# Optimization experiments

Hardware: AMD Instinct MI355X
Metric: run time of the kernel (lower is better)

The kernel has to match this reference:

```python
import jax, jax.numpy as jnp
import numpy as np
from jax.scipy.linalg import expm

N, T, IN, C, M = 64, 2048, 8, 2, 10  # batch, time, input_size, channels, hidden_size


def setup_inputs() -> dict:
    key = jax.random.key(0)
    k1, k2 = jax.random.split(key)
    x = jax.random.normal(k1, (N, T, IN), dtype=jnp.float32)
    # Lie-algebra generator parameters; small init keeps expm well-conditioned
    A = jax.random.normal(k2, (C, IN, M, M), dtype=jnp.float32) * (1.0 / (M * IN))
    return {"x": x, "A": A}


def dyadic_prod(X):
    # X: (N, T, C, m, m) -> cumulative (ordered) matrix product over time: (N, C, m, m)
    n, t, c, m, _ = X.shape
    levels = int(np.ceil(np.log2(t)))
    I = jnp.broadcast_to(jnp.eye(m, dtype=X.dtype), (n, 1, c, m, m))
    for _ in range(levels):
        if X.shape[1] % 2 == 1:
            X = jnp.concatenate([X, I], axis=1)  # pad with identity
        Xp = X.reshape(n, -1, 2, c, m, m)
        X = jnp.einsum('ntcij,ntcjk->ntcik', Xp[:, :, 0], Xp[:, :, 1])
    return X[:, 0]


def reference(x, A):
    # Skew-symmetrize generators -> so(m) Lie algebra elements, per channel/input dim
    skew = A - jnp.swapaxes(A, -1, -2)          # (C, IN, m, m)
    dX = x[:, 1:] - x[:, :-1]                   # (N, T-1, IN) path increments
    G = jnp.einsum('nti,cijk->ntcjk', dX, skew) # (N, T-1, C, m, m)
    Mexp = expm(G)                              # batched matrix exponential -> SO(m)
    return dyadic_prod(Mexp)                    # (N, C, m, m)
```

## Files before the change

### kernel.cpp

```cpp
#include <hip/hip_runtime.h>

#define NB     64
#define TT     2048
#define INQ    8
#define CC     2
#define MM     10
#define ROWP   12
#define MATS   124
#define SKST   12
#define BLK    512
#define SEGS   96
#define SLEN   11
#define NCHK   2
#define NCHAIN (NB*CC)
#define SLOT   120

typedef float v2f __attribute__((ext_vector_type(2)));

static_assert(SEGS * MATS >= 97 * SLOT, "scratch overlay must fit tree buffer");

__device__ __forceinline__ constexpr int triIdx(int k, int j) {
    return k * 10 + j - ((k + 1) * (k + 2)) / 2;
}

__device__ __forceinline__ void trow_pk(const float* __restrict__ Tri,
                                        v2f* A, v2f* R, const v2f* S, float cj) {
    v2f t[MM];
    t[0] = -S[1] * Tri[triIdx(0, 1)];
    #pragma unroll
    for (int j = 1; j < MM; ++j) t[j] = S[0] * Tri[triIdx(0, j)];
    #pragma unroll
    for (int k = 1; k < MM; ++k) {
        const v2f a = S[k];
        #pragma unroll
        for (int j = 0; j < MM; ++j) {
            if (k == j) continue;
            if (j == 0 && k == 1) continue;
            if (j > k) t[j] += a * Tri[triIdx(k, j)];
            else       t[j] -= a * Tri[triIdx(j, k)];
        }
    }
    #pragma unroll
    for (int j = 0; j < MM; ++j) { A[j] = t[j]; R[j] += cj * t[j]; }
}

__device__ __forceinline__ void taylor5(const float* __restrict__ Tri, v2f* R01) {
    __builtin_amdgcn_s_setprio(1);
    v2f A01[MM];
    trow_pk(Tri, A01, R01, R01, 1.0f);
    trow_pk(Tri, A01, R01, A01, 0.5f);
    trow_pk(Tri, A01, R01, A01, 0.16666667f);
    trow_pk(Tri, A01, R01, A01, 0.041666668f);
    trow_pk(Tri, A01, R01, A01, 0.0083333338f);
    __builtin_amdgcn_s_setprio(0);
}

__device__ __forceinline__ void compute_tvv(const float4* __restrict__ px, int t,
                                            const float4* __restrict__ sg,
                                            float* __restrict__ tvv) {
    const int tc = (t     > TT - 1) ? TT - 1 : t;
    const int t1 = (t + 1 > TT - 1) ? TT - 1 : t + 1;
    const float4 a0 = px[2 * tc], a1 = px[2 * tc + 1];
    const float4 b0 = px[2 * t1], b1 = px[2 * t1 + 1];
    float dx[INQ];
    dx[0] = b0.x - a0.x; dx[1] = b0.y - a0.y;
    dx[2] = b0.z - a0.z; dx[3] = b0.w - a0.w;
    dx[4] = b1.x - a1.x; dx[5] = b1.y - a1.y;
    dx[6] = b1.z - a1.z; dx[7] = b1.w - a1.w;
    #pragma unroll
    for (int i = 0; i < 9; ++i) {
        const float4 s0 = sg[2 * i];
        const float4 s1 = sg[2 * i + 1];
        tvv[i] = dx[0] * s0.x + dx[1] * s0.y + dx[2] * s0.z + dx[3] * s0.w
               + dx[4] * s1.x + dx[5] * s1.y + dx[6] * s1.z + dx[7] * s1.w;
    }
}

__device__ __forceinline__ void store_tvv(float* __restrict__ dst, int r,
                                          const float* __restrict__ tvv) {
    *reinterpret_cast<float4*>(dst + 12 * r)     = make_float4(tvv[0], tvv[1], tvv[2], tvv[3]);
    *reinterpret_cast<float4*>(dst + 12 * r + 4) = make_float4(tvv[4], tvv[5], tvv[6], tvv[7]);
    dst[12 * r + 8] = tvv[8];
}

__device__ __forceinline__ void load_tri(const float* __restrict__ src,
                                         float* __restrict__ Tri) {
    #pragma unroll
    for (int q2 = 0; q2 < 5; ++q2) {
        const float4 u0 = *reinterpret_cast<const float4*>(src + 12 * q2);
        const float4 u1 = *reinterpret_cast<const float4*>(src + 12 * q2 + 4);
        const float  u2 = src[12 * q2 + 8];
        Tri[9 * q2 + 0] = u0.x; Tri[9 * q2 + 1] = u0.y;
        Tri[9 * q2 + 2] = u0.z; Tri[9 * q2 + 3] = u0.w;
        Tri[9 * q2 + 4] = u1.x; Tri[9 * q2 + 5] = u1.y;
        Tri[9 * q2 + 6] = u1.z; Tri[9 * q2 + 7] = u1.w;
        Tri[9 * q2 + 8] = u2;
    }
}

__device__ __forceinline__ void pair_combine(float* buf_s, int ls, int rs, int pq) {
    float lrow[5][MM];
    #pragma unroll
    for (int r = 0; r < 5; ++r) {
        const float4* lr = reinterpret_cast<const float4*>(
            &buf_s[ls * MATS + (pq * 5 + r) * ROWP]);
        const float4 a = lr[0], b = lr[1], c4 = lr[2];
        lrow[r][0] = a.x;  lrow[r][1] = a.y;  lrow[r][2] = a.z;  lrow[r][3] = a.w;
        lrow[r][4] = b.x;  lrow[r][5] = b.y;  lrow[r][6] = b.z;  lrow[r][7] = b.w;
        lrow[r][8] = c4.x; lrow[r][9] = c4.y;
    }
    float d[5][MM];
    #pragma unroll
    for (int r = 0; r < 5; ++r)
        #pragma unroll
        for (int j = 0; j < MM; ++j)
            d[r][j] = 0.0f;
    #pragma unroll
    for (int k = 0; k < MM; ++k) {
        const float4* rr = reinterpret_cast<const float4*>(&buf_s[rs * MATS + k * ROWP]);
        const float4 a = rr[0], b = rr[1], c4 = rr[2];
        float rrow[MM];
        rrow[0] = a.x;  rrow[1] = a.y;  rrow[2] = a.z;  rrow[3] = a.w;
        rrow[4] = b.x;  rrow[5] = b.y;  rrow[6] = b.z;  rrow[7] = b.w;
        rrow[8] = c4.x; rrow[9] = c4.y;
        #pragma unroll
        for (int r = 0; r < 5; ++r) {
            const float lv = lrow[r][k];
            #pragma unroll
            for (int j = 0; j < MM; ++j)
                d[r][j] += lv * rrow[j];
        }
    }
    float* dst = &buf_s[ls * MATS + pq * 5 * ROWP];
    #pragma unroll
    for (int r = 0; r < 5; ++r) {
        float4* drow = reinterpret_cast<float4*>(dst + r * ROWP);
        drow[0] = make_float4(d[r][0], d[r][1], d[r][2], d[r][3]);
        drow[1] = make_float4(d[r][4], d[r][5], d[r][6], d[r][7]);
        drow[2] = make_float4(d[r][8], d[r][9], 0.0f, 0.0f);
    }
}

__global__ __launch_bounds__(BLK, 1)
void dev_serial(const float* __restrict__ x,
                const float* __restrict__ A,
                float* __restrict__ ws)
{
    __shared__ __align__(16) float skq_s[45 * SKST];
    __shared__ __align__(16) float buf_s[SEGS * MATS];

    const int tid   = threadIdx.x;
    const int chain = blockIdx.x >> 1;
    const int qt    = blockIdx.x & 1;
    const int n     = chain >> 1;
    const int c     = chain & 1;

    if (tid < 45 * 8) {
        const int e  = tid >> 3;
        const int ip = tid & 7;
        int k = 0, r2 = e;
        while (r2 >= 9 - k) { r2 -= (9 - k); ++k; }
        const int j = k + 1 + r2;
        const float* Ab = A + (size_t)(c * INQ + ip) * (MM * MM);
        skq_s[e * SKST + ip] = Ab[k * MM + j] - Ab[j * MM + k];
    }
    __syncthreads();

    const int wv  = tid >> 6;
    const int wl  = tid & 63;
    const int g   = wl / 5;
    const int r   = wl - 5 * g;
    const bool act = (wl < 60);
    const int seg = wv * 12 + g;
    const int p0  = 2 * r;

    float4 sg[18];
    {
        const float* srow = &skq_s[(9 * r) * SKST];
        #pragma unroll
        for (int i = 0; i < 9; ++i) {
            sg[2 * i]     = *reinterpret_cast<const float4*>(srow + i * SKST);
            sg[2 * i + 1] = *reinterpret_cast<const float4*>(srow + i * SKST + 4);
        }
    }

    float* slot  = &buf_s[seg * SLOT];
    float* slotw = act ? slot : &buf_s[96 * SLOT];

    v2f R01[MM];
    #pragma unroll
    for (int j = 0; j < MM; ++j)
        R01[j] = (v2f){ (j == p0) ? 1.0f : 0.0f, (j == p0 + 1) ? 1.0f : 0.0f };

    const float4* px = reinterpret_cast<const float4*>(x + (size_t)n * TT * INQ);
    const int t0 = qt * (SEGS * SLEN) + seg * SLEN;

    float tvv[9];
    compute_tvv(px, t0, sg, tvv);
    store_tvv(slotw, r, tvv);

    #pragma unroll 1
    for (int s = 0; s < SLEN - 1; ++s) {
        const int rpar = (s & 1) * 60;
        float Tri[45];
        load_tri(slot + rpar, Tri);
        compute_tvv(px, t0 + s + 1, sg, tvv);
        store_tvv(slotw + (60 - rpar), r, tvv);
        taylor5(Tri, R01);
    }
    {
        float Tri[45];
        load_tri(slot + ((SLEN - 1) & 1) * 60, Tri);
        taylor5(Tri, R01);
    }

    __syncthreads();

    if (act) {
        float* dst = &buf_s[seg * MATS];
        float4* d0 = reinterpret_cast<float4*>(dst + p0 * ROWP);
        d0[0] = make_float4(R01[0].x, R01[1].x, R01[2].x, R01[3].x);
        d0[1] = make_float4(R01[4].x, R01[5].x, R01[6].x, R01[7].x);
        d0[2] = make_float4(R01[8].x, R01[9].x, 0.0f, 0.0f);
        float4* d1 = reinterpret_cast<float4*>(dst + (p0 + 1) * ROWP);
        d1[0] = make_float4(R01[0].y, R01[1].y, R01[2].y, R01[3].y);
        d1[1] = make_float4(R01[4].y, R01[5].y, R01[6].y, R01[7].y);
        d1[2] = make_float4(R01[8].y, R01[9].y, 0.0f, 0.0f);
    }
    __syncthreads();

    #pragma unroll 1
    for (int span = 2; span <= 32; span <<= 1) {
        const int np = SEGS / span;
        if (tid < 2 * np) {
            const int pr = tid >> 1;
            const int pq = tid & 1;
            pair_combine(buf_s, pr * span, pr * span + (span >> 1), pq);
        }
        __syncthreads();
    }
    if (tid < 2) pair_combine(buf_s, 0, 32, tid);
    __syncthreads();
    if (tid < 2) pair_combine(buf_s, 0, 64, tid);
    __syncthreads();

    if (tid < 30) {
        const float4 v = reinterpret_cast<const float4*>(buf_s)[tid];
        reinterpret_cast<float4*>(ws)[((size_t)chain * NCHK + qt) * 30 + tid] = v;
    }
}

__global__ __launch_bounds__(256)
void dev_tree2(const float* __restrict__ ws, float* __restrict__ out)
{
    __shared__ __align__(16) float buf_s[2 * MATS];
    const int tid   = threadIdx.x;
    const int chain = blockIdx.x;

    if (tid < 60) {
        const int m  = tid / 30;
        const int o4 = tid - m * 30;
        const float4 v = reinterpret_cast<const float4*>(ws)[((size_t)chain * 2 + m) * 30 + o4];
        reinterpret_cast<float4*>(&buf_s[m * MATS])[o4] = v;
    }
    __syncthreads();

    if (tid < 2)
        pair_combine(buf_s, 0, 1, tid);
    __syncthreads();

    if (tid < 100) {
        const int i = tid / 10;
        const int j = tid - i * 10;
        out[(size_t)chain * 100 + tid] = buf_s[i * ROWP + j];
    }
}

extern "C" void kernel_launch(void* const* d_in, const int* in_sizes, int n_in,
                              void* d_out, int out_size, void* d_ws, size_t ws_size,
                              hipStream_t stream) {
    (void)in_sizes; (void)n_in; (void)out_size; (void)ws_size;
    const float* x = (const float*)d_in[0];
    const float* A = (const float*)d_in[1];
    float* out = (float*)d_out;
    float* ws  = (float*)d_ws;

    dev_serial<<<dim3(NCHAIN * NCHK), dim3(BLK), 0, stream>>>(x, A, ws);
    dev_tree2<<<dim3(NCHAIN), dim3(256), 0, stream>>>(ws, out);
}
```

Before: 93.28 us.

## Process two segments per thread group with interleaved Taylor chains

Halves the block to 256 threads and has each 5-lane group carry two time segments, interleaving their Taylor-5 matrix-exponential updates for more instruction-level parallelism. The scratch layout is regrouped into 240-float slots holding both segments' generator triangles. Launch bounds drop the min-blocks hint, so two blocks may share a CU. The cost is doubled register pressure from two sets of Tri, A and R arrays, which may cause spills or lower occupancy.

Result: slower. 98.19 us (+5.3%).

```diff
diff --git a/kernel.cpp b/kernel.cpp
--- a/kernel.cpp
+++ b/kernel.cpp
@@ -8,16 +8,16 @@
 #define ROWP   12
 #define MATS   124
 #define SKST   12
-#define BLK    512
+#define BLK    256
 #define SEGS   96
 #define SLEN   11
 #define NCHK   2
 #define NCHAIN (NB*CC)
-#define SLOT   120
+#define GSLOT  240
 
 typedef float v2f __attribute__((ext_vector_type(2)));
 
-static_assert(SEGS * MATS >= 97 * SLOT, "scratch overlay must fit tree buffer");
+static_assert(SEGS * MATS >= 49 * GSLOT, "scratch overlay must fit tree buffer");
 
 __device__ __forceinline__ constexpr int triIdx(int k, int j) {
     return k * 10 + j - ((k + 1) * (k + 2)) / 2;
@@ -44,14 +44,20 @@
     for (int j = 0; j < MM; ++j) { A[j] = t[j]; R[j] += cj * t[j]; }
 }
 
-__device__ __forceinline__ void taylor5(const float* __restrict__ Tri, v2f* R01) {
+__device__ __forceinline__ void taylor5_dual(const float* __restrict__ TriA, v2f* RA,
+                                             const float* __restrict__ TriB, v2f* RB) {
     __builtin_amdgcn_s_setprio(1);
-    v2f A01[MM];
-    trow_pk(Tri, A01, R01, R01, 1.0f);
-    trow_pk(Tri, A01, R01, A01, 0.5f);
-    trow_pk(Tri, A01, R01, A01, 0.16666667f);
-    trow_pk(Tri, A01, R01, A01, 0.041666668f);
-    trow_pk(Tri, A01, R01, A01, 0.0083333338f);
+    v2f Aa[MM], Ab[MM];
+    trow_pk(TriA, Aa, RA, RA, 1.0f);
+    trow_pk(TriB, Ab, RB, RB, 1.0f);
+    trow_pk(TriA, Aa, RA, Aa, 0.5f);
+    trow_pk(TriB, Ab, RB, Ab, 0.5f);
+    trow_pk(TriA, Aa, RA, Aa, 0.16666667f);
+    trow_pk(TriB, Ab, RB, Ab, 0.16666667f);
+    trow_pk(TriA, Aa, RA, Aa, 0.041666668f);
+    trow_pk(TriB, Ab, RB, Ab, 0.041666668f);
+    trow_pk(TriA, Aa, RA, Aa, 0.0083333338f);
+    trow_pk(TriB, Ab, RB, Ab, 0.0083333338f);
     __builtin_amdgcn_s_setprio(0);
 }
 
@@ -141,7 +147,7 @@
     }
 }
 
-__global__ __launch_bounds__(BLK, 1)
+__global__ __launch_bounds__(BLK)
 void dev_serial(const float* __restrict__ x,
                 const float* __restrict__ A,
                 float* __restrict__ ws)
@@ -155,9 +161,9 @@
     const int n     = chain >> 1;
     const int c     = chain & 1;
 
-    if (tid < 45 * 8) {
-        const int e  = tid >> 3;
-        const int ip = tid & 7;
+    for (int e4 = tid; e4 < 45 * 8; e4 += BLK) {
+        const int e  = e4 >> 3;
+        const int ip = e4 & 7;
         int k = 0, r2 = e;
         while (r2 >= 9 - k) { r2 -= (9 - k); ++k; }
         const int j = k + 1 + r2;
@@ -171,7 +177,9 @@
     const int g   = wl / 5;
     const int r   = wl - 5 * g;
     const bool act = (wl < 60);
-    const int seg = wv * 12 + g;
+    const int grp = wv * 12 + g;
+    const int segA = grp * 2;
+    const int segB = grp * 2 + 1;
     const int p0  = 2 * r;
 
     float4 sg[18];
@@ -184,48 +192,67 @@
         }
     }
 
-    float* slot  = &buf_s[seg * SLOT];
-    float* slotw = act ? slot : &buf_s[96 * SLOT];
-
-    v2f R01[MM];
-    #pragma unroll
-    for (int j = 0; j < MM; ++j)
-        R01[j] = (v2f){ (j == p0) ? 1.0f : 0.0f, (j == p0 + 1) ? 1.0f : 0.0f };
+    float* slot  = &buf_s[grp * GSLOT];
+    float* slotw = act ? slot : &buf_s[48 * GSLOT];
+
+    v2f RA[MM], RB[MM];
+    #pragma unroll
+    for (int j = 0; j < MM; ++j) {
+        RA[j] = (v2f){ (j == p0) ? 1.0f : 0.0f, (j == p0 + 1) ? 1.0f : 0.0f };
+        RB[j] = RA[j];
+    }
 
     const float4* px = reinterpret_cast<const float4*>(x + (size_t)n * TT * INQ);
-    const int t0 = qt * (SEGS * SLEN) + seg * SLEN;
-
-    float tvv[9];
-    compute_tvv(px, t0, sg, tvv);
-    store_tvv(slotw, r, tvv);
+    const int t0A = qt * (SEGS * SLEN) + segA * SLEN;
+    const int t0B = t0A + SLEN;
+
+    float tvvA[9], tvvB[9];
+    compute_tvv(px, t0A, sg, tvvA);
+    compute_tvv(px, t0B, sg, tvvB);
+    store_tvv(slotw,       r, tvvA);
+    store_tvv(slotw + 120, r, tvvB);
 
     #pragma unroll 1
     for (int s = 0; s < SLEN - 1; ++s) {
         const int rpar = (s & 1) * 60;
-        float Tri[45];
-        load_tri(slot + rpar, Tri);
-        compute_tvv(px, t0 + s + 1, sg, tvv);
-        store_tvv(slotw + (60 - rpar), r, tvv);
-        taylor5(Tri, R01);
+        float TriA[45], TriB[45];
+        load_tri(slot + rpar,       TriA);
+        load_tri(slot + 120 + rpar, TriB);
+        compute_tvv(px, t0A + s + 1, sg, tvvA);
+        compute_tvv(px, t0B + s + 1, sg, tvvB);
+        store_tvv(slotw + (60 - rpar),       r, tvvA);
+        store_tvv(slotw + 120 + (60 - rpar), r, tvvB);
+        taylor5_dual(TriA, RA, TriB, RB);
     }
     {
-        float Tri[45];
-        load_tri(slot + ((SLEN - 1) & 1) * 60, Tri);
-        taylor5(Tri, R01);
+        const int rpar = ((SLEN - 1) & 1) * 60;
+        float TriA[45], TriB[45];
+        load_tri(slot + rpar,       TriA);
+        load_tri(slot + 120 + rpar, TriB);
+        taylor5_dual(TriA, RA, TriB, RB);
     }
 
     __syncthreads();
 
     if (act) {
-        float* dst = &buf_s[seg * MATS];
-        float4* d0 = reinterpret_cast<float4*>(dst + p0 * ROWP);
-        d0[0] = make_float4(R01[0].x, R01[1].x, R01[2].x, R01[3].x);
-        d0[1] = make_float4(R01[4].x, R01[5].x, R01[6].x, R01[7].x);
-        d0[2] = make_float4(R01[8].x, R01[9].x, 0.0f, 0.0f);
-        float4* d1 = reinterpret_cast<float4*>(dst + (p0 + 1) * ROWP);
-        d1[0] = make_float4(R01[0].y, R01[1].y, R01[2].y, R01[3].y);
-        d1[1] = make_float4(R01[4].y, R01[5].y, R01[6].y, R01[7].y);
-        d1[2] = make_float4(R01[8].y, R01[9].y, 0.0f, 0.0f);
+        float* dstA = &buf_s[segA * MATS];
+        float4* a0 = reinterpret_cast<float4*>(dstA + p0 * ROWP);
+        a0[0] = make_float4(RA[0].x, RA[1].x, RA[2].x, RA[3].x);
+        a0[1] = make_float4(RA[4].x, RA[5].x, RA[6].x, RA[7].x);
+        a0[2] = make_float4(RA[8].x, RA[9].x, 0.0f, 0.0f);
+        float4* a1 = reinterpret_cast<float4*>(dstA + (p0 + 1) * ROWP);
+        a1[0] = make_float4(RA[0].y, RA[1].y, RA[2].y, RA[3].y);
+        a1[1] = make_float4(RA[4].y, RA[5].y, RA[6].y, RA[7].y);
+        a1[2] = make_float4(RA[8].y, RA[9].y, 0.0f, 0.0f);
+        float* dstB = &buf_s[segB * MATS];
+        float4* b0 = reinterpret_cast<float4*>(dstB + p0 * ROWP);
+        b0[0] = make_float4(RB[0].x, RB[1].x, RB[2].x, RB[3].x);
+        b0[1] = make_float4(RB[4].x, RB[5].x, RB[6].x, RB[7].x);
+        b0[2] = make_float4(RB[8].x, RB[9].x, 0.0f, 0.0f);
+        float4* b1 = reinterpret_cast<float4*>(dstB + (p0 + 1) * ROWP);
+        b1[0] = make_float4(RB[0].y, RB[1].y, RB[2].y, RB[3].y);
+        b1[1] = make_float4(RB[4].y, RB[5].y, RB[6].y, RB[7].y);
+        b1[2] = make_float4(RB[8].y, RB[9].y, 0.0f, 0.0f);
     }
     __syncthreads();
 
```
